# Optimization experiments

Hardware: AMD Instinct MI355X
Metric: run time of the kernel (lower is better)

The kernel has to match this reference:

```python
import jax, jax.numpy as jnp
import numpy as np

BB_MIN = -2.0
BB_MAX = 2.0
GRID_RES = 256
VOXEL_SIZE = (BB_MAX - BB_MIN) / (GRID_RES - 1)
# corner order matches torch code x1..x8: (dx,dy,dz) with dx outer, dz inner
CORNERS = [(dx, dy, dz) for dx in (0, 1) for dy in (0, 1) for dz in (0, 1)]


def _grid_normals(g, vs):
    # central differences interior, one-sided extrapolated boundary (as in get_grid_normal)
    def axis_normal(ax):
        n = g.shape[ax] - 1
        sl = lambda a, b: jax.lax.slice_in_dim(g, a, b, axis=ax)
        hi = (3 * sl(n, n + 1) - sl(n - 2, n - 1)) / 2
        lo = (3 * sl(0, 1) - sl(2, 3)) / 2
        fwd = jnp.concatenate([sl(1, n + 1), hi], axis=ax)
        bwd = jnp.concatenate([lo, sl(0, n)], axis=ax)
        return (fwd - bwd) / (2 * vs)
    return axis_normal(0), axis_normal(1), axis_normal(2)


def _gather8(gn, x, y, z):
    # flat index = z + R*y + R*R*x, 8 voxel corners -> [H, W, 8]
    flat = gn.reshape(-1)
    idx = jnp.stack([(z + dz) + GRID_RES * (y + dy) + GRID_RES * GRID_RES * (x + dx)
                     for dx, dy, dz in CORNERS], axis=-1)
    return jnp.take(flat, idx)


def _trilinear(c, tx, ty, tz):
    # weight order matches get_intersection_normal
    w = jnp.stack([
        (1 - tz) * (1 - ty) * (1 - tx), tz * (1 - ty) * (1 - tx),
        (1 - tz) * ty * (1 - tx),       tz * ty * (1 - tx),
        (1 - tz) * (1 - ty) * tx,       tz * (1 - ty) * tx,
        (1 - tz) * ty * tx,             tz * ty * tx], axis=-1)
    return jnp.sum(c * w, axis=-1)


def setup_inputs() -> dict:
    key = jax.random.key(0)
    k0, k1, k2, k3 = jax.random.split(key, 4)
    H, W = 400, 3200
    grid = jax.random.normal(k0, (GRID_RES, GRID_RES, GRID_RES), dtype=jnp.float32) * 0.1
    voxel_idx = jax.random.randint(k1, (H, W, 3), 0, GRID_RES - 1)  # <=254, +1 stays in-range
    voxel_min_point = BB_MIN + voxel_idx.astype(jnp.float32) * VOXEL_SIZE
    intersection_pos = voxel_min_point + jax.random.uniform(k2, (H, W, 3), dtype=jnp.float32) * VOXEL_SIZE
    mask = jax.random.randint(k3, (H, W), 0, 2)
    return {"grid": grid, "voxel_idx": voxel_idx, "intersection_pos": intersection_pos,
            "voxel_min_point": voxel_min_point, "mask": mask}


def reference(grid, voxel_idx, intersection_pos, voxel_min_point, mask):
    nx, ny, nz = _grid_normals(grid, VOXEL_SIZE)
    x = voxel_idx[..., 0]
    y = voxel_idx[..., 1]
    z = voxel_idx[..., 2]
    m = mask.astype(grid.dtype)
    t = (intersection_pos - voxel_min_point) / VOXEL_SIZE
    tx, ty, tz = t[..., 0], t[..., 1], t[..., 2]
    inv = (1 - m)[..., None]  # masked-out rays get +1 on all 8 corners (as in source)
    normals = jnp.stack([
        _trilinear(_gather8(gn, x, y, z) + inv, tx, ty, tz)
        for gn in (nx, ny, nz)], axis=-1)  # [H, W, 3]
    # relu(-grid) value gather at the base corner, zeroed where mask==0
    gridx = jnp.take(jax.nn.relu(-grid).reshape(-1),
                     z + GRID_RES * y + GRID_RES * GRID_RES * x) * m
    return jnp.concatenate([normals, gridx[..., None]], axis=-1)  # [H, W, 4]
```

## Files before the change

kernel.cpp:

```cpp
#include <hip/hip_runtime.h>
#include <hip/hip_bf16.h>

#define GRID_R   256
#define GRID_RR  65536
#define NVOX     16777216
#define NBRK     128
#define INV_2VS  31.875f
#define INV_VS   63.75f
#define VSF      0.015686275f

__device__ __forceinline__ float h2f(unsigned short u) {
    union { unsigned short s; _Float16 f; } cv; cv.s = u; return (float)cv.f;
}
__device__ __forceinline__ unsigned f2h2(float a, float b) {
    union { unsigned short s; _Float16 f; } ca, cb;
    ca.f = (_Float16)a; cb.f = (_Float16)b;
    return (unsigned)ca.s | ((unsigned)cb.s << 16);
}


__global__ __launch_bounds__(256) void precompute_tile_kernel(
    const float* __restrict__ grid,
    uint2*       __restrict__ packed)
{
    __shared__ float ls[10*10*40];
    __shared__ uint4 lout[256*4];

    const int bid = blockIdx.x;
    const int t   = threadIdx.x;
    const int tz  = bid & 7;
    const int ty  = (bid >> 3) & 31;
    const int tx  = bid >> 8;
    const int xt0 = tx << 3, yt0 = ty << 3, zt0 = tz << 5;

    #pragma unroll
    for (int it = 0; it < 4; ++it) {
        int w = t + (it << 8);
        if (w < 1000) {
            int lx  = w / 100;
            int rem = w - lx * 100;
            int ly  = rem / 10;
            int seg = rem - ly * 10;
            int gx = min(max(xt0 - 1 + lx, 0), 255);
            int gy = min(max(yt0 - 1 + ly, 0), 255);
            int zb = min(max(zt0 - 4 + (seg << 2), 0), 252);
            float4 v = *reinterpret_cast<const float4*>(
                grid + (gx << 16) + (gy << 8) + zb);
            *reinterpret_cast<float4*>(&ls[(lx * 10 + ly) * 40 + (seg << 2)]) = v;
        }
    }
    __syncthreads();

    const int lbz = t & 15, lby = (t >> 4) & 3, lbx = t >> 6;
    const int Lx = lbx << 1, Ly = lby << 1, Lz = lbz << 1;
    #define S(ix,iy,iz) ls[((1 + Lx + (ix)) * 10 + (1 + Ly + (iy))) * 40 + (4 + Lz + (iz))]

    float c[2][2][2], xlo[2][2], xhi[2][2], ylo[2][2], yhi[2][2], zlo[2][2], zhi[2][2];
    #pragma unroll
    for (int dy = 0; dy < 2; ++dy)
    #pragma unroll
    for (int dz = 0; dz < 2; ++dz) { xlo[dy][dz] = S(-1, dy, dz); xhi[dy][dz] = S(2, dy, dz); }
    #pragma unroll
    for (int dx = 0; dx < 2; ++dx)
    #pragma unroll
    for (int dz = 0; dz < 2; ++dz) { ylo[dx][dz] = S(dx, -1, dz); yhi[dx][dz] = S(dx, 2, dz); }
    #pragma unroll
    for (int dx = 0; dx < 2; ++dx)
    #pragma unroll
    for (int dy = 0; dy < 2; ++dy) { zlo[dx][dy] = S(dx, dy, -1); zhi[dx][dy] = S(dx, dy, 2); }
    #pragma unroll
    for (int dx = 0; dx < 2; ++dx)
    #pragma unroll
    for (int dy = 0; dy < 2; ++dy)
    #pragma unroll
    for (int dz = 0; dz < 2; ++dz) c[dx][dy][dz] = S(dx, dy, dz);
    #undef S

    const int x0 = xt0 + Lx, y0 = yt0 + Ly, z0 = zt0 + Lz;
    const bool xb0 = (x0 == 0), xb1 = (x0 + 1 == 255);
    const bool yb0 = (y0 == 0), yb1 = (y0 + 1 == 255);
    const bool zb0 = (z0 == 0), zb1 = (z0 + 1 == 255);

    uint2 slot[8];
    #pragma unroll
    for (int dx = 0; dx < 2; ++dx)
    #pragma unroll
    for (int dy = 0; dy < 2; ++dy)
    #pragma unroll
    for (int dz = 0; dz < 2; ++dz) {
        float g0 = c[dx][dy][dz];

        float nx;
        if (xb0 && dx == 0)      nx = (c[1][dy][dz] - 1.5f*g0 + 0.5f*xhi[dy][dz]) * INV_2VS;
        else if (xb1 && dx == 1) nx = (1.5f*g0 - 0.5f*xlo[dy][dz] - c[0][dy][dz]) * INV_2VS;
        else nx = ((dx ? xhi[dy][dz] : c[1][dy][dz]) - (dx ? c[0][dy][dz] : xlo[dy][dz])) * INV_2VS;

        float ny;
        if (yb0 && dy == 0)      ny = (c[dx][1][dz] - 1.5f*g0 + 0.5f*yhi[dx][dz]) * INV_2VS;
        else if (yb1 && dy == 1) ny = (1.5f*g0 - 0.5f*ylo[dx][dz] - c[dx][0][dz]) * INV_2VS;
        else ny = ((dy ? yhi[dx][dz] : c[dx][1][dz]) - (dy ? c[dx][0][dz] : ylo[dx][dz])) * INV_2VS;

        float nz;
        if (zb0 && dz == 0)      nz = (c[dx][dy][1] - 1.5f*g0 + 0.5f*zhi[dx][dy]) * INV_2VS;
        else if (zb1 && dz == 1) nz = (1.5f*g0 - 0.5f*zlo[dx][dy] - c[dx][dy][0]) * INV_2VS;
        else nz = ((dz ? zhi[dx][dy] : c[dx][dy][1]) - (dz ? c[dx][dy][0] : zlo[dx][dy])) * INV_2VS;

        int s = dx*4 + dy*2 + dz;
        slot[s].x = f2h2(nx, ny);
        slot[s].y = f2h2(nz, g0);
    }

    #pragma unroll
    for (int j = 0; j < 4; ++j) {
        uint4 st; st.x = slot[2*j].x;   st.y = slot[2*j].y;
                  st.z = slot[2*j+1].x; st.w = slot[2*j+1].y;
        lout[t*4 + j] = st;
    }
    __syncthreads();

    const int chunk = t >> 4;
    const int idx   = t & 15;
    const int cbx = (tx << 2) + (chunk >> 2);
    const int cby = (ty << 2) + (chunk & 3);
    const long long Bg = ((long long)(cbx * NBRK + cby)) * NBRK + (tz << 4);
    uint4*       gdst = reinterpret_cast<uint4*>(packed) + Bg * 4;
    const uint4* lsrc = &lout[chunk << 6];
    #pragma unroll
    for (int j = 0; j < 4; ++j)
        gdst[idx + (j << 4)] = lsrc[idx + (j << 4)];
}

__global__ __launch_bounds__(256) void gather_kernel(
    const uint2* __restrict__ packed,
    const int*   __restrict__ vidx,
    const float* __restrict__ ipos,
    const int*   __restrict__ mask,
    float*       __restrict__ out,
    int n)
{
    int i = blockIdx.x * blockDim.x + threadIdx.x;
    if (i >= n) return;

    int x = vidx[3*i+0];
    int y = vidx[3*i+1];
    int z = vidx[3*i+2];

    float tx = (ipos[3*i+0] - (-2.0f + (float)x * VSF)) * INV_VS;
    float ty = (ipos[3*i+1] - (-2.0f + (float)y * VSF)) * INV_VS;
    float tz = (ipos[3*i+2] - (-2.0f + (float)z * VSF)) * INV_VS;

    int   m   = mask[i];
    float inv = 1.0f - (float)m;

    float ox = 1.0f - tx, oy = 1.0f - ty, oz = 1.0f - tz;
    float w[8];
    w[0] = oz*oy*ox;  w[1] = tz*oy*ox;  w[2] = oz*ty*ox;  w[3] = tz*ty*ox;
    w[4] = oz*oy*tx;  w[5] = tz*oy*tx;  w[6] = oz*ty*tx;  w[7] = tz*ty*tx;

    float accx = 0.f, accy = 0.f, accz = 0.f;
    float gbase = 0.f;

    #pragma unroll
    for (int k = 0; k < 8; ++k) {
        int cx = x + (k >> 2), cy = y + ((k >> 1) & 1), cz = z + (k & 1);
        int B  = ((cx >> 1)*NBRK + (cy >> 1))*NBRK + (cz >> 1);
        int s  = (cx & 1)*4 + (cy & 1)*2 + (cz & 1);
        uint2 p = packed[B*8 + s];
        accx += h2f(p.x & 0xffff) * w[k];
        accy += h2f(p.x >> 16)    * w[k];
        accz += h2f(p.y & 0xffff) * w[k];
        if (k == 0) gbase = h2f(p.y >> 16);
    }

    float4 o;
    o.x = accx + inv;
    o.y = accy + inv;
    o.z = accz + inv;
    o.w = fmaxf(-gbase, 0.0f) * (float)m;
    *reinterpret_cast<float4*>(out + 4*i) = o;
}

__global__ __launch_bounds__(256) void sdf_grid_kernel(
    const float* __restrict__ grid,
    const int*   __restrict__ vidx,
    const float* __restrict__ ipos,
    const float* __restrict__ vmin,
    const int*   __restrict__ mask,
    float*       __restrict__ out,
    int n)
{
    int i = blockIdx.x * blockDim.x + threadIdx.x;
    if (i >= n) return;
    int x = vidx[3*i+0], y = vidx[3*i+1], z = vidx[3*i+2];
    float tx = (ipos[3*i+0] - vmin[3*i+0]) * INV_VS;
    float ty = (ipos[3*i+1] - vmin[3*i+1]) * INV_VS;
    float tz = (ipos[3*i+2] - vmin[3*i+2]) * INV_VS;
    int   m   = mask[i];
    float inv = 1.0f - (float)m;
    float ox = 1.0f - tx, oy = 1.0f - ty, oz = 1.0f - tz;
    float w[8];
    w[0] = oz*oy*ox;  w[1] = tz*oy*ox;  w[2] = oz*ty*ox;  w[3] = tz*ty*ox;
    w[4] = oz*oy*tx;  w[5] = tz*oy*tx;  w[6] = oz*ty*tx;  w[7] = tz*ty*tx;
    int base = z + GRID_R*y + GRID_RR*x;
    float nout[3];
    #pragma unroll
    for (int a = 0; a < 3; ++a) {
        const int s  = (a==0) ? GRID_RR : (a==1) ? GRID_R : 1;
        const int c0 = (a==0) ? x : (a==1) ? y : z;
        float acc = 0.0f;
        #pragma unroll
        for (int k = 0; k < 8; ++k) {
            const int dx = k>>2, dy = (k>>1)&1, dz = k&1;
            const int b  = base + dz + GRID_R*dy + GRID_RR*dx;
            const int cc = c0 + ((a==0) ? dx : (a==1) ? dy : dz);
            float v;
            if (cc == 0)            v = grid[b+s] - (3.0f*grid[b] - grid[b+2*s])*0.5f;
            else if (cc == GRID_R-1) v = (3.0f*grid[b] - grid[b-2*s])*0.5f - grid[b-s];
            else                    v = grid[b+s] - grid[b-s];
            acc += (v*INV_2VS + inv) * w[k];
        }
        nout[a] = acc;
    }
    float gx = fmaxf(-grid[base], 0.0f) * (float)m;
    float4 o; o.x = nout[0]; o.y = nout[1]; o.z = nout[2]; o.w = gx;
    *reinterpret_cast<float4*>(out + 4*i) = o;
}

extern "C" void kernel_launch(void* const* d_in, const int* in_sizes, int n_in,
                              void* d_out, int out_size, void* d_ws, size_t ws_size,
                              hipStream_t stream) {
    const float* grid = (const float*)d_in[0];
    const int*   vidx = (const int*)d_in[1];
    const float* ipos = (const float*)d_in[2];
    const float* vmin = (const float*)d_in[3];
    const int*   mask = (const int*)d_in[4];
    float*       out  = (float*)d_out;

    const int n = in_sizes[4];
    const int block = 256;

    if (ws_size >= (size_t)NVOX * 8) {
        uint2* packed = (uint2*)d_ws;
        precompute_tile_kernel<<<8192, block, 0, stream>>>(grid, packed);
        gather_kernel<<<(n + block - 1) / block, block, 0, stream>>>(
            packed, vidx, ipos, mask, out, n);
    } else {
        sdf_grid_kernel<<<(n + block - 1) / block, block, 0, stream>>>(
            grid, vidx, ipos, vmin, mask, out, n);
    }
}
```

Before: 236.5 us.

## Replace LDS-tiled normal precompute with per-thread z-column streaming kernel

The precompute kernel is rewritten so each thread walks a 32-voxel z column segment, reading its neighbour columns straight from global memory with float4 loads and no shared-memory staging or barriers. The packed fp16 normal/value layout is kept, but it is now written straight from registers. The goal is to drop the halo overhead and LDS round trips of the 8x8x32 tile approach. In exchange it relies on L2/cache reuse for neighbour columns, may produce less coalesced stores, and launches fewer blocks.

After: 292.2 us. 23.5% more time.

```diff
diff --git a/kernel.cpp b/kernel.cpp
--- a/kernel.cpp
+++ b/kernel.cpp
@@ -19,115 +19,99 @@
 }
 
 
-__global__ __launch_bounds__(256) void precompute_tile_kernel(
+__global__ __launch_bounds__(256) void precompute_col_kernel(
     const float* __restrict__ grid,
     uint2*       __restrict__ packed)
 {
-    __shared__ float ls[10*10*40];
-    __shared__ uint4 lout[256*4];
-
+    const int t   = threadIdx.x;
     const int bid = blockIdx.x;
-    const int t   = threadIdx.x;
-    const int tz  = bid & 7;
-    const int ty  = (bid >> 3) & 31;
-    const int tx  = bid >> 8;
-    const int xt0 = tx << 3, yt0 = ty << 3, zt0 = tz << 5;
+    const int zseg  = bid & 7;
+    const int patch = bid >> 3;
+    const int Xb = (patch >> 4) << 4;
+    const int Yb = (patch & 15) << 4;
+
+    const int dx = (t >> 1) & 1;
+    const int dy = t & 1;
+    const int bq = t >> 2;
+    const int pbx = bq >> 3, pby = bq & 7;
+    const int x = Xb + (pbx << 1) + dx;
+    const int y = Yb + (pby << 1) + dy;
+
+    const bool xlo = (x == 0), xhi = (x == 255);
+    const bool ylo = (y == 0), yhi = (y == 255);
+    const bool xbd = xlo || xhi, ybd = ylo || yhi;
+
+    const float* colC  = grid + (x << 16) + (y << 8);
+    const float* colXm = grid + (max(x - 1, 0)   << 16) + (y << 8);
+    const float* colXp = grid + (min(x + 1, 255) << 16) + (y << 8);
+    const float* colYm = grid + (x << 16) + (max(y - 1, 0)   << 8);
+    const float* colYp = grid + (x << 16) + (min(y + 1, 255) << 8);
+    const float* colX2 = grid + ((xlo ? 2 : 253) << 16) + (y << 8);
+    const float* colY2 = grid + (x << 16) + ((ylo ? 2 : 253) << 8);
+
+    const int j0 = zseg << 3;
+    float4 cur = *reinterpret_cast<const float4*>(colC + (j0 << 2));
+    float prevlast = (j0 > 0) ? colC[(j0 << 2) - 1] : 0.0f;
+
+    const int gbx = x >> 1, gby = y >> 1;
+    uint4* outp = reinterpret_cast<uint4*>(packed)
+                + ((((gbx << 7) + gby) << 7) + (j0 << 1)) * 4 + ((dx << 1) + dy);
 
     #pragma unroll
-    for (int it = 0; it < 4; ++it) {
-        int w = t + (it << 8);
-        if (w < 1000) {
-            int lx  = w / 100;
-            int rem = w - lx * 100;
-            int ly  = rem / 10;
-            int seg = rem - ly * 10;
-            int gx = min(max(xt0 - 1 + lx, 0), 255);
-            int gy = min(max(yt0 - 1 + ly, 0), 255);
-            int zb = min(max(zt0 - 4 + (seg << 2), 0), 252);
-            float4 v = *reinterpret_cast<const float4*>(
-                grid + (gx << 16) + (gy << 8) + zb);
-            *reinterpret_cast<float4*>(&ls[(lx * 10 + ly) * 40 + (seg << 2)]) = v;
+    for (int jj = 0; jj < 8; ++jj) {
+        const int j  = j0 + jj;
+        const int jn = (j < 63) ? j + 1 : 63;
+        const float4 nxt = *reinterpret_cast<const float4*>(colC  + (jn << 2));
+        const float4 vxm = *reinterpret_cast<const float4*>(colXm + (j  << 2));
+        const float4 vxp = *reinterpret_cast<const float4*>(colXp + (j  << 2));
+        const float4 vym = *reinterpret_cast<const float4*>(colYm + (j  << 2));
+        const float4 vyp = *reinterpret_cast<const float4*>(colYp + (j  << 2));
+        float4 vx2 = make_float4(0.f, 0.f, 0.f, 0.f);
+        float4 vy2 = make_float4(0.f, 0.f, 0.f, 0.f);
+        if (xbd) vx2 = *reinterpret_cast<const float4*>(colX2 + (j << 2));
+        if (ybd) vy2 = *reinterpret_cast<const float4*>(colY2 + (j << 2));
+
+        const float cw[6]  = {prevlast, cur.x, cur.y, cur.z, cur.w, nxt.x};
+        const float axm[4] = {vxm.x, vxm.y, vxm.z, vxm.w};
+        const float axp[4] = {vxp.x, vxp.y, vxp.z, vxp.w};
+        const float aym[4] = {vym.x, vym.y, vym.z, vym.w};
+        const float ayp[4] = {vyp.x, vyp.y, vyp.z, vyp.w};
+        const float ax2[4] = {vx2.x, vx2.y, vx2.z, vx2.w};
+        const float ay2[4] = {vy2.x, vy2.y, vy2.z, vy2.w};
+
+        unsigned h[8];
+        #pragma unroll
+        for (int q = 0; q < 4; ++q) {
+            const int z = (j << 2) + q;
+            const float g0 = cw[q + 1];
+
+            float nx;
+            if (xlo)      nx = (axp[q] - 1.5f*g0 + 0.5f*ax2[q]) * INV_2VS;
+            else if (xhi) nx = (1.5f*g0 - 0.5f*ax2[q] - axm[q]) * INV_2VS;
+            else          nx = (axp[q] - axm[q]) * INV_2VS;
+
+            float ny;
+            if (ylo)      ny = (ayp[q] - 1.5f*g0 + 0.5f*ay2[q]) * INV_2VS;
+            else if (yhi) ny = (1.5f*g0 - 0.5f*ay2[q] - aym[q]) * INV_2VS;
+            else          ny = (ayp[q] - aym[q]) * INV_2VS;
+
+            float nz;
+            if (z == 0)        nz = (cw[2] - 1.5f*cw[1] + 0.5f*cw[3]) * INV_2VS;
+            else if (z == 255) nz = (1.5f*cw[4] - 0.5f*cw[2] - cw[3]) * INV_2VS;
+            else               nz = (cw[q + 2] - cw[q]) * INV_2VS;
+
+            h[2*q]     = f2h2(nx, ny);
+            h[2*q + 1] = f2h2(nz, g0);
         }
-    }
-    __syncthreads();
-
-    const int lbz = t & 15, lby = (t >> 4) & 3, lbx = t >> 6;
-    const int Lx = lbx << 1, Ly = lby << 1, Lz = lbz << 1;
-    #define S(ix,iy,iz) ls[((1 + Lx + (ix)) * 10 + (1 + Ly + (iy))) * 40 + (4 + Lz + (iz))]
-
-    float c[2][2][2], xlo[2][2], xhi[2][2], ylo[2][2], yhi[2][2], zlo[2][2], zhi[2][2];
-    #pragma unroll
-    for (int dy = 0; dy < 2; ++dy)
-    #pragma unroll
-    for (int dz = 0; dz < 2; ++dz) { xlo[dy][dz] = S(-1, dy, dz); xhi[dy][dz] = S(2, dy, dz); }
-    #pragma unroll
-    for (int dx = 0; dx < 2; ++dx)
-    #pragma unroll
-    for (int dz = 0; dz < 2; ++dz) { ylo[dx][dz] = S(dx, -1, dz); yhi[dx][dz] = S(dx, 2, dz); }
-    #pragma unroll
-    for (int dx = 0; dx < 2; ++dx)
-    #pragma unroll
-    for (int dy = 0; dy < 2; ++dy) { zlo[dx][dy] = S(dx, dy, -1); zhi[dx][dy] = S(dx, dy, 2); }
-    #pragma unroll
-    for (int dx = 0; dx < 2; ++dx)
-    #pragma unroll
-    for (int dy = 0; dy < 2; ++dy)
-    #pragma unroll
-    for (int dz = 0; dz < 2; ++dz) c[dx][dy][dz] = S(dx, dy, dz);
-    #undef S
-
-    const int x0 = xt0 + Lx, y0 = yt0 + Ly, z0 = zt0 + Lz;
-    const bool xb0 = (x0 == 0), xb1 = (x0 + 1 == 255);
-    const bool yb0 = (y0 == 0), yb1 = (y0 + 1 == 255);
-    const bool zb0 = (z0 == 0), zb1 = (z0 + 1 == 255);
-
-    uint2 slot[8];
-    #pragma unroll
-    for (int dx = 0; dx < 2; ++dx)
-    #pragma unroll
-    for (int dy = 0; dy < 2; ++dy)
-    #pragma unroll
-    for (int dz = 0; dz < 2; ++dz) {
-        float g0 = c[dx][dy][dz];
-
-        float nx;
-        if (xb0 && dx == 0)      nx = (c[1][dy][dz] - 1.5f*g0 + 0.5f*xhi[dy][dz]) * INV_2VS;
-        else if (xb1 && dx == 1) nx = (1.5f*g0 - 0.5f*xlo[dy][dz] - c[0][dy][dz]) * INV_2VS;
-        else nx = ((dx ? xhi[dy][dz] : c[1][dy][dz]) - (dx ? c[0][dy][dz] : xlo[dy][dz])) * INV_2VS;
-
-        float ny;
-        if (yb0 && dy == 0)      ny = (c[dx][1][dz] - 1.5f*g0 + 0.5f*yhi[dx][dz]) * INV_2VS;
-        else if (yb1 && dy == 1) ny = (1.5f*g0 - 0.5f*ylo[dx][dz] - c[dx][0][dz]) * INV_2VS;
-        else ny = ((dy ? yhi[dx][dz] : c[dx][1][dz]) - (dy ? c[dx][0][dz] : ylo[dx][dz])) * INV_2VS;
-
-        float nz;
-        if (zb0 && dz == 0)      nz = (c[dx][dy][1] - 1.5f*g0 + 0.5f*zhi[dx][dy]) * INV_2VS;
-        else if (zb1 && dz == 1) nz = (1.5f*g0 - 0.5f*zlo[dx][dy] - c[dx][dy][0]) * INV_2VS;
-        else nz = ((dz ? zhi[dx][dy] : c[dx][dy][1]) - (dz ? c[dx][dy][0] : zlo[dx][dy])) * INV_2VS;
-
-        int s = dx*4 + dy*2 + dz;
-        slot[s].x = f2h2(nx, ny);
-        slot[s].y = f2h2(nz, g0);
-    }
-
-    #pragma unroll
-    for (int j = 0; j < 4; ++j) {
-        uint4 st; st.x = slot[2*j].x;   st.y = slot[2*j].y;
-                  st.z = slot[2*j+1].x; st.w = slot[2*j+1].y;
-        lout[t*4 + j] = st;
-    }
-    __syncthreads();
-
-    const int chunk = t >> 4;
-    const int idx   = t & 15;
-    const int cbx = (tx << 2) + (chunk >> 2);
-    const int cby = (ty << 2) + (chunk & 3);
-    const long long Bg = ((long long)(cbx * NBRK + cby)) * NBRK + (tz << 4);
-    uint4*       gdst = reinterpret_cast<uint4*>(packed) + Bg * 4;
-    const uint4* lsrc = &lout[chunk << 6];
-    #pragma unroll
-    for (int j = 0; j < 4; ++j)
-        gdst[idx + (j << 4)] = lsrc[idx + (j << 4)];
+
+        uint4 s0; s0.x = h[0]; s0.y = h[1]; s0.z = h[2]; s0.w = h[3];
+        uint4 s1; s1.x = h[4]; s1.y = h[5]; s1.z = h[6]; s1.w = h[7];
+        outp[(jj << 3)]     = s0;
+        outp[(jj << 3) + 4] = s1;
+
+        prevlast = cur.w;
+        cur = nxt;
+    }
 }
 
 __global__ __launch_bounds__(256) void gather_kernel(
@@ -241,7 +225,7 @@
 
     if (ws_size >= (size_t)NVOX * 8) {
         uint2* packed = (uint2*)d_ws;
-        precompute_tile_kernel<<<8192, block, 0, stream>>>(grid, packed);
+        precompute_col_kernel<<<2048, block, 0, stream>>>(grid, packed);
         gather_kernel<<<(n + block - 1) / block, block, 0, stream>>>(
             packed, vidx, ipos, mask, out, n);
     } else {
```
